# Optimization experiments

Hardware: AMD Instinct MI355X
Metric: run time of the kernel (lower is better)

The kernel has to match this reference:

```python
import jax, jax.numpy as jnp
import numpy as np

B, S, HID = 2, 2048, 4096
NUM_HEADS, NUM_KV_HEADS, HEAD_DIM = 32, 8, 128
KV_SIZE = HID * NUM_KV_HEADS // NUM_HEADS  # 1024


def setup_inputs() -> dict:
    key = jax.random.key(0)
    ks = jax.random.split(key, 5)
    x = jax.random.normal(ks[0], (B, S, HID), dtype=jnp.float32)
    wq = jax.random.normal(ks[1], (HID, HID), dtype=jnp.float32) * 0.02
    wk = jax.random.normal(ks[2], (HID, KV_SIZE), dtype=jnp.float32) * 0.02
    wv = jax.random.normal(ks[3], (HID, KV_SIZE), dtype=jnp.float32) * 0.02
    wo = jax.random.normal(ks[4], (KV_SIZE, HID), dtype=jnp.float32) * 0.02
    return {"x": x, "wq": wq, "wk": wk, "wv": wv, "wo": wo}


def reference(x, wq, wk, wv, wo):
    b, s, _ = x.shape
    g = NUM_HEADS // NUM_KV_HEADS  # num_head_groups
    q = x @ wq  # [b, s, hid]
    k = x @ wk  # [b, s, kv_size]
    v = x @ wv  # [b, s, kv_size]
    # 'b s (h d) -> b h s d' with h = num_heads
    q = q.reshape(b, s, NUM_HEADS, HEAD_DIM).transpose(0, 2, 1, 3)
    # 'b s (h d) -> b h d s' with h = num_kv_heads
    k = k.reshape(b, s, NUM_KV_HEADS, HEAD_DIM).transpose(0, 2, 3, 1)
    # 'b s (h d) -> b h s d'
    v = v.reshape(b, s, NUM_KV_HEADS, HEAD_DIM).transpose(0, 2, 1, 3)
    # 'b (h g) s d -> b g h s d' with g = num_head_groups, h = num_kv_heads
    q = q.reshape(b, NUM_KV_HEADS, g, s, HEAD_DIM).transpose(0, 2, 1, 3, 4)
    # NOTE: faithful to source - g is contracted (summed) here, it does not
    # appear in the output subscripts.
    scores = jnp.einsum('bghqd,bhdk->bhqk', q, k) / jnp.sqrt(
        jnp.asarray(HEAD_DIM, dtype=x.dtype))
    scores = jax.nn.softmax(scores, axis=-1)
    values = jnp.einsum('bhqk,bhkd->bhqd', scores, v)  # [b, h_kv, s, d]
    values = values.transpose(0, 2, 1, 3).reshape(b, s, KV_SIZE)
    return values @ wo  # [b, s, hid]
```

## Files before the change

kernel.cpp:

```cpp
#include <hip/hip_runtime.h>
#include <stdint.h>

#define S 2048
#define HID 4096
#define NKV 8
#define HD 128
#define KV 1024
#define BATCH 2
#define NQKV 3072
#define MROWS 4096

typedef __attribute__((ext_vector_type(4))) float f32x4;
typedef __attribute__((ext_vector_type(8))) __bf16 bf16x8;
typedef __attribute__((ext_vector_type(8))) unsigned short ushort8;
typedef __attribute__((ext_vector_type(4))) unsigned short ushort4_t;
typedef __attribute__((ext_vector_type(4))) float float4_t;

__device__ __forceinline__ unsigned short f2bf(float f) {
    unsigned int u = __builtin_bit_cast(unsigned int, f);
    u += 0x7fffu + ((u >> 16) & 1u);
    return (unsigned short)(u >> 16);
}
__device__ __forceinline__ float bf2f(unsigned short s) {
    unsigned int u = ((unsigned int)s) << 16;
    return __builtin_bit_cast(float, u);
}

__device__ __forceinline__ void gl2lds16(const void* g, void* l) {
    __builtin_amdgcn_global_load_lds(
        (const __attribute__((address_space(1))) void*)(uintptr_t)(g),
        (__attribute__((address_space(3))) void*)(uintptr_t)(l),
        16, 0, 0);
}

__global__ __launch_bounds__(256) void castx_kernel(const float* __restrict__ x,
                                                    unsigned short* __restrict__ xb) {
    int i = (blockIdx.x * 256 + threadIdx.x) * 4;
    float4_t v = *(const float4_t*)&x[i];
    ushort4_t o;
    o.x = f2bf(v.x); o.y = f2bf(v.y); o.z = f2bf(v.z); o.w = f2bf(v.w);
    *(ushort4_t*)&xb[i] = o;
}

__global__ __launch_bounds__(256) void wcat_kernel(const float* __restrict__ wq,
                                                   const float* __restrict__ wk,
                                                   const float* __restrict__ wv,
                                                   unsigned short* __restrict__ WcatT) {
    __shared__ float T[64 * 65];
    const int tid = threadIdx.x;
    const int k0 = blockIdx.x * 64;
    const int n0 = blockIdx.y * 64;
    const float scale = 0.088388347648318447f;
#pragma unroll
    for (int i = 0; i < 16; i++) {
        int kl = (tid >> 6) + i * 4;
        int nl = tid & 63;
        int k = k0 + kl, n = n0 + nl;
        float v;
        if (n < KV) {
            int kvh = n >> 7, d = n & 127;
            const float* p = wq + (size_t)k * HID + kvh * 512 + d;
            v = (p[0] + p[128] + p[256] + p[384]) * scale;
        } else if (n < 2048) {
            v = wk[(size_t)k * KV + (n - KV)];
        } else {
            v = wv[(size_t)k * KV + (n - 2048)];
        }
        T[kl * 65 + nl] = v;
    }
    __syncthreads();
#pragma unroll
    for (int i = 0; i < 16; i++) {
        int nl = (tid >> 6) + i * 4;
        int kl = tid & 63;
        WcatT[(size_t)(n0 + nl) * HID + k0 + kl] = f2bf(T[kl * 65 + nl]);
    }
}

__global__ __launch_bounds__(256) void wot_kernel(const float* __restrict__ wo,
                                                  unsigned short* __restrict__ woT) {
    __shared__ float T[64 * 65];
    const int tid = threadIdx.x;
    const int k0 = blockIdx.x * 64;
    const int n0 = blockIdx.y * 64;
#pragma unroll
    for (int i = 0; i < 16; i++) {
        int kl = (tid >> 6) + i * 4, nl = tid & 63;
        T[kl * 65 + nl] = wo[(size_t)(k0 + kl) * HID + n0 + nl];
    }
    __syncthreads();
#pragma unroll
    for (int i = 0; i < 16; i++) {
        int nl = (tid >> 6) + i * 4, kl = tid & 63;
        woT[(size_t)(n0 + nl) * KV + k0 + kl] = f2bf(T[kl * 65 + nl]);
    }
}

#define BAR() do { asm volatile("" ::: "memory"); __builtin_amdgcn_s_barrier(); asm volatile("" ::: "memory"); } while (0)
#define WAITV2() asm volatile("s_waitcnt vmcnt(2)" ::: "memory")

__device__ __forceinline__ void stage2(const unsigned short* __restrict__ g,
                                       size_t so0, size_t so1,
                                       unsigned short* lds, int tid) {
    gl2lds16(g + so0, lds + (size_t)tid * 8);
    gl2lds16(g + so1, lds + (size_t)(512 + tid) * 8);
}

template <int OUT_BF16>
__global__ __launch_bounds__(512, 2) void gemm_bt8(const unsigned short* __restrict__ A,
                                                   const unsigned short* __restrict__ Bt,
                                                   void* __restrict__ Cv,
                                                   int M, int N, int K) {
    __shared__ unsigned short As[2][2][8192];
    __shared__ unsigned short Bs[2][2][8192];
    const int tid = threadIdx.x;
    const int lane = tid & 63, wave = tid >> 6;
    const int lm = lane & 15, quad = lane >> 4;
    const int wm = wave >> 2;
    const int wn = wave & 3;
    const int wnh = wn >> 1;
    const int wnb = (wn & 1) * 4;

    const int nbx = gridDim.x;
    const int id = blockIdx.y * nbx + blockIdx.x;
    const int cpx = (nbx * gridDim.y) >> 3;
    const int sid = (id & 7) * cpx + (id >> 3);
    const int m0 = (sid / nbx) * 256;
    const int n0 = (sid % nbx) * 256;

    size_t so0, so1;
    {
#pragma unroll
        for (int i = 0; i < 2; i++) {
            int p = i * 512 + tid;
            int ps = p ^ (((p >> 5) & 1) << 1);
            int s = ps >> 6, w = ps & 63;
            int row = ((s >> 1) << 4) + (w >> 2);
            int kc = ((s & 1) << 5) + ((w & 3) << 3);
            size_t off = (size_t)row * K + kc;
            if (i == 0) so0 = off; else so1 = off;
        }
    }
    const unsigned short* Agb = A + (size_t)m0 * K;
    const unsigned short* Bgb = Bt + (size_t)n0 * K;
    const size_t hK = (size_t)128 * K;

    const int roff = lm * 32 + ((quad << 3) ^ (((lm >> 3) & 1) << 4));

#define LDA(mi, kk, BUF) a[(mi) & 3][kk] = *(const bf16x8*)&As[BUF][wm][(((mi) * 2 + (kk)) << 9) + roff]
#define LDB(ni, kk, BUF) b[ni][kk] = *(const bf16x8*)&Bs[BUF][wnh][(((wnb + (ni)) * 2 + (kk)) << 9) + roff]
#define RD_A_LO(BUF) { LDA(0,0,BUF); LDA(0,1,BUF); LDA(1,0,BUF); LDA(1,1,BUF); LDA(2,0,BUF); LDA(2,1,BUF); LDA(3,0,BUF); LDA(3,1,BUF); }
#define RD_A_HI(BUF) { LDA(4,0,BUF); LDA(4,1,BUF); LDA(5,0,BUF); LDA(5,1,BUF); LDA(6,0,BUF); LDA(6,1,BUF); LDA(7,0,BUF); LDA(7,1,BUF); }
#define RD_B_LO(BUF) { LDB(0,0,BUF); LDB(0,1,BUF); LDB(1,0,BUF); LDB(1,1,BUF); }
#define RD_B_HI(BUF) { LDB(2,0,BUF); LDB(2,1,BUF); LDB(3,0,BUF); LDB(3,1,BUF); }
#define MFMA_Q(MB, NB) do { \
    __builtin_amdgcn_s_setprio(1); \
    _Pragma("unroll") for (int i_ = 0; i_ < 4; i_++) \
    _Pragma("unroll") for (int j_ = 0; j_ < 2; j_++) \
    _Pragma("unroll") for (int k_ = 0; k_ < 2; k_++) \
        acc[(MB) + i_][(NB) + j_] = __builtin_amdgcn_mfma_f32_16x16x32_bf16( \
            a[i_][k_], b[(NB) + j_][k_], acc[(MB) + i_][(NB) + j_], 0, 0, 0); \
    __builtin_amdgcn_s_setprio(0); \
} while (0)

    f32x4 acc[8][4] = {};
    bf16x8 a[4][2], b[4][2];

    const int KT = K >> 6;
    const int NT = KT >> 1;

    stage2(Agb, so0, so1, &As[0][0][0], tid);
    stage2(Agb + hK, so0, so1, &As[0][1][0], tid);
    stage2(Bgb, so0, so1, &Bs[0][0][0], tid);
    stage2(Bgb + hK, so0, so1, &Bs[0][1][0], tid);
    stage2(Agb + 64, so0, so1, &As[1][0][0], tid);
    WAITV2();
    BAR();

    for (int t = 0; t < NT; ++t) {
        const int t1 = 2 * t + 1;
        int t2 = 2 * t + 2; if (t2 >= KT) t2 = KT - 1;
        int t3 = 2 * t + 3; if (t3 >= KT) t3 = KT - 1;
        const size_t k1 = (size_t)t1 * 64, k2 = (size_t)t2 * 64, k3 = (size_t)t3 * 64;

        RD_A_LO(0); RD_B_LO(0);
        stage2(Agb + hK + k1, so0, so1, &As[1][1][0], tid);
        BAR(); MFMA_Q(0, 0); BAR();

        RD_B_HI(0);
        stage2(Bgb + k1, so0, so1, &Bs[1][0][0], tid);
        BAR(); MFMA_Q(0, 2); BAR();

        RD_A_HI(0);
        stage2(Bgb + hK + k1, so0, so1, &Bs[1][1][0], tid);
        BAR(); MFMA_Q(4, 2); BAR();

        stage2(Agb + k2, so0, so1, &As[0][0][0], tid);
        BAR(); MFMA_Q(4, 0);
        WAITV2();
        BAR();

        RD_A_LO(1); RD_B_LO(1);
        stage2(Agb + hK + k2, so0, so1, &As[0][1][0], tid);
        BAR(); MFMA_Q(0, 0); BAR();

        RD_B_HI(1);
        stage2(Bgb + k2, so0, so1, &Bs[0][0][0], tid);
        BAR(); MFMA_Q(0, 2); BAR();

        RD_A_HI(1);
        stage2(Bgb + hK + k2, so0, so1, &Bs[0][1][0], tid);
        BAR(); MFMA_Q(4, 2); BAR();

        stage2(Agb + k3, so0, so1, &As[1][0][0], tid);
        BAR(); MFMA_Q(4, 0);
        WAITV2();
        BAR();
    }

    const int crow0 = m0 + wm * 128 + quad * 4;
    const int ccol0 = n0 + wn * 64 + lm;
#pragma unroll
    for (int mi = 0; mi < 8; mi++)
#pragma unroll
        for (int ni = 0; ni < 4; ni++)
#pragma unroll
            for (int r = 0; r < 4; r++) {
                const int row = crow0 + mi * 16 + r;
                const int col = ccol0 + ni * 16;
                if (OUT_BF16)
                    ((unsigned short*)Cv)[(size_t)row * N + col] = f2bf(acc[mi][ni][r]);
                else
                    ((float*)Cv)[(size_t)row * N + col] = acc[mi][ni][r];
            }
#undef LDA
#undef LDB
#undef RD_A_LO
#undef RD_A_HI
#undef RD_B_LO
#undef RD_B_HI
#undef MFMA_Q
}

__global__ __launch_bounds__(256) void vt_kernel(const unsigned short* __restrict__ QKV,
                                                 unsigned short* __restrict__ Vt) {
    __shared__ unsigned short T[128 * 136];
    const int tid = threadIdx.x;
    const int st = blockIdx.x;
    const int bh = blockIdx.y;
    const int b = bh >> 3, h = bh & 7;
#pragma unroll
    for (int it = 0; it < 8; it++) {
        int chunk = tid + it * 256;
        int s = chunk >> 4, cc = chunk & 15;
        ushort8 v = *(const ushort8*)&QKV[(size_t)(b * S + st * 128 + s) * NQKV + 2048 + h * HD + cc * 8];
        *(ushort8*)&T[s * 136 + cc * 8] = v;
    }
    __syncthreads();
#pragma unroll
    for (int it = 0; it < 8; it++) {
        int chunk = tid + it * 256;
        int d = chunk >> 4, scc = chunk & 15;
        ushort8 o;
#pragma unroll
        for (int j = 0; j < 8; j++) o[j] = T[(scc * 8 + j) * 136 + d];
        *(ushort8*)&Vt[(size_t)((b * NKV + h) * HD + d) * S + st * 128 + scc * 8] = o;
    }
}

__global__ __launch_bounds__(256, 1) void attn_kernel(const unsigned short* __restrict__ QKV,
                                                      const unsigned short* __restrict__ Vt,
                                                      unsigned short* __restrict__ Oout) {
    __shared__ unsigned short Ks[64 * 128];
    __shared__ unsigned short Vs[128 * 64];
    __shared__ unsigned short Ps[128 * 64];
    const int tid = threadIdx.x;
    const int lane = tid & 63, wave = tid >> 6;
    const int lm = lane & 15, quad = lane >> 4;
    const int sw = lm & 7;
    const int qt = blockIdx.x;
    const int h = blockIdx.y;
    const int b = blockIdx.z;
    const int qrow0 = qt * 128 + wave * 32;

    bf16x8 qf[2][4];
#pragma unroll
    for (int rt = 0; rt < 2; rt++)
#pragma unroll
        for (int ks = 0; ks < 4; ks++) {
            size_t off = (size_t)(b * S + qrow0 + rt * 16 + lm) * NQKV + h * HD + ks * 32 + quad * 8;
            qf[rt][ks] = *(const bf16x8*)&QKV[off];
        }

    float lsum[2][4] = {};
    f32x4 oacc[2][8] = {};

    const int krow = tid >> 2, kc4 = tid & 3;
    const int vrow = tid >> 1, vc2 = tid & 1;
    const unsigned short* Kg0 = QKV + (size_t)(b * S) * NQKV + KV + h * HD + kc4 * 32;
    const unsigned short* Vg0 = Vt + (size_t)((b * NKV + h) * HD + vrow) * S + vc2 * 32;

    ushort8 kreg[4], vreg[4];
    {
        const unsigned short* kg = Kg0 + (size_t)krow * NQKV;
        const unsigned short* vg = Vg0;
#pragma unroll
        for (int j = 0; j < 4; j++) kreg[j] = *(const ushort8*)(kg + j * 8);
#pragma unroll
        for (int j = 0; j < 4; j++) vreg[j] = *(const ushort8*)(vg + j * 8);
    }

    for (int kt = 0; kt < 32; kt++) {
        __syncthreads();
#pragma unroll
        for (int j = 0; j < 4; j++)
            *(ushort8*)&Ks[krow * 128 + ((kc4 * 4 + j) ^ (krow & 7)) * 8] = kreg[j];
#pragma unroll
        for (int j = 0; j < 4; j++)
            *(ushort8*)&Vs[vrow * 64 + ((vc2 * 4 + j) ^ (vrow & 7)) * 8] = vreg[j];
        __syncthreads();
        if (kt < 31) {
            const unsigned short* kg = Kg0 + (size_t)((kt + 1) * 64 + krow) * NQKV;
            const unsigned short* vg = Vg0 + (kt + 1) * 64;
#pragma unroll
            for (int j = 0; j < 4; j++) kreg[j] = *(const ushort8*)(kg + j * 8);
#pragma unroll
            for (int j = 0; j < 4; j++) vreg[j] = *(const ushort8*)(vg + j * 8);
        }

        f32x4 sc[2][4] = {};
#pragma unroll
        for (int ks = 0; ks < 4; ks++)
#pragma unroll
            for (int ct = 0; ct < 4; ct++) {
                bf16x8 kf = *(const bf16x8*)&Ks[(ct * 16 + lm) * 128 + ((ks * 4 + quad) ^ sw) * 8];
                sc[0][ct] = __builtin_amdgcn_mfma_f32_16x16x32_bf16(qf[0][ks], kf, sc[0][ct], 0, 0, 0);
                sc[1][ct] = __builtin_amdgcn_mfma_f32_16x16x32_bf16(qf[1][ks], kf, sc[1][ct], 0, 0, 0);
            }

#pragma unroll
        for (int rt = 0; rt < 2; rt++)
#pragma unroll
            for (int ct = 0; ct < 4; ct++)
#pragma unroll
                for (int r = 0; r < 4; r++) {
                    float p = __expf(fminf(sc[rt][ct][r], 60.f));
                    unsigned short pb = f2bf(p);
                    lsum[rt][r] += bf2f(pb);
                    int prow = wave * 32 + rt * 16 + quad * 4 + r;
                    int pcol = ct * 16 + lm;
                    Ps[prow * 64 + (((pcol >> 3) ^ (prow & 7)) * 8) + (pcol & 7)] = pb;
                }

#pragma unroll
        for (int ks = 0; ks < 2; ks++) {
            bf16x8 af0 = *(const bf16x8*)&Ps[(wave * 32 + lm) * 64 + ((ks * 4 + quad) ^ sw) * 8];
            bf16x8 af1 = *(const bf16x8*)&Ps[(wave * 32 + 16 + lm) * 64 + ((ks * 4 + quad) ^ sw) * 8];
#pragma unroll
            for (int dt = 0; dt < 8; dt++) {
                bf16x8 vf = *(const bf16x8*)&Vs[(dt * 16 + lm) * 64 + ((ks * 4 + quad) ^ sw) * 8];
                oacc[0][dt] = __builtin_amdgcn_mfma_f32_16x16x32_bf16(af0, vf, oacc[0][dt], 0, 0, 0);
                oacc[1][dt] = __builtin_amdgcn_mfma_f32_16x16x32_bf16(af1, vf, oacc[1][dt], 0, 0, 0);
            }
        }
    }

#pragma unroll
    for (int rt = 0; rt < 2; rt++)
#pragma unroll
        for (int r = 0; r < 4; r++) {
            float v = lsum[rt][r];
            v += __shfl_xor(v, 8);
            v += __shfl_xor(v, 4);
            v += __shfl_xor(v, 2);
            v += __shfl_xor(v, 1);
            lsum[rt][r] = v;
        }
#pragma unroll
    for (int rt = 0; rt < 2; rt++)
#pragma unroll
        for (int dt = 0; dt < 8; dt++)
#pragma unroll
            for (int r = 0; r < 4; r++) {
                int row = b * S + qt * 128 + wave * 32 + rt * 16 + quad * 4 + r;
                int col = h * HD + dt * 16 + lm;
                Oout[(size_t)row * KV + col] = f2bf(oacc[rt][dt][r] / lsum[rt][r]);
            }
}

extern "C" void kernel_launch(void* const* d_in, const int* in_sizes, int n_in,
                              void* d_out, int out_size, void* d_ws, size_t ws_size,
                              hipStream_t stream) {
    (void)in_sizes; (void)n_in; (void)out_size; (void)ws_size;
    const float* x  = (const float*)d_in[0];
    const float* wq = (const float*)d_in[1];
    const float* wk = (const float*)d_in[2];
    const float* wv = (const float*)d_in[3];
    const float* wo = (const float*)d_in[4];
    float* out = (float*)d_out;
    char* ws = (char*)d_ws;

    unsigned short* xb    = (unsigned short*)(ws);
    unsigned short* WcatT = (unsigned short*)(ws + 33554432);
    unsigned short* woT   = (unsigned short*)(ws + 33554432 + 25165824);
    unsigned short* QKV   = (unsigned short*)(ws + 67108864);
    unsigned short* Vt    = (unsigned short*)(ws);
    unsigned short* AttnO = (unsigned short*)(ws + 8388608);

    castx_kernel<<<16384, 256, 0, stream>>>(x, xb);
    wcat_kernel<<<dim3(64, 48), 256, 0, stream>>>(wq, wk, wv, WcatT);
    wot_kernel<<<dim3(16, 64), 256, 0, stream>>>(wo, woT);
    gemm_bt8<1><<<dim3(NQKV / 256, MROWS / 256), 512, 0, stream>>>(xb, WcatT, QKV, MROWS, NQKV, HID);
    vt_kernel<<<dim3(16, 16), 256, 0, stream>>>(QKV, Vt);
    attn_kernel<<<dim3(16, NKV, BATCH), 256, 0, stream>>>(QKV, Vt, AttnO);
    gemm_bt8<0><<<dim3(HID / 256, MROWS / 256), 512, 0, stream>>>(AttnO, woT, out, MROWS, HID, KV);
}
```

Baseline: 426.3 us.

## Reorder GEMM prefetch into half-tile stages and shrink attention query tile to 64 rows

The GEMM load schedule is reorganised so each stage issues the lo/hi halves of A and B across both 128-row halves, with a deeper prefetch (vmcnt(6)) so more global-to-LDS traffic is in flight while MFMAs run. Separately, the attention kernel now processes 64 query rows per block (16 per wave) instead of 128, which doubles the grid to 512 blocks and raises occupancy to 2 blocks per CU with a smaller P buffer. The cost is that each loaded K/V tile is reused by fewer query rows, so K/V traffic doubles, and the reordered wait counts must stay correct for the ring of LDS buffers.

```diff
diff --git a/kernel.cpp b/kernel.cpp
--- a/kernel.cpp
+++ b/kernel.cpp
@@ -97,14 +97,7 @@
 }
 
 #define BAR() do { asm volatile("" ::: "memory"); __builtin_amdgcn_s_barrier(); asm volatile("" ::: "memory"); } while (0)
-#define WAITV2() asm volatile("s_waitcnt vmcnt(2)" ::: "memory")
-
-__device__ __forceinline__ void stage2(const unsigned short* __restrict__ g,
-                                       size_t so0, size_t so1,
-                                       unsigned short* lds, int tid) {
-    gl2lds16(g + so0, lds + (size_t)tid * 8);
-    gl2lds16(g + so1, lds + (size_t)(512 + tid) * 8);
-}
+#define WAITV6() asm volatile("s_waitcnt vmcnt(6)" ::: "memory")
 
 template <int OUT_BF16>
 __global__ __launch_bounds__(512, 2) void gemm_bt8(const unsigned short* __restrict__ A,
@@ -144,6 +137,9 @@
     const unsigned short* Agb = A + (size_t)m0 * K;
     const unsigned short* Bgb = Bt + (size_t)n0 * K;
     const size_t hK = (size_t)128 * K;
+
+#define STLO(G, L) gl2lds16((G) + so0, (L) + (size_t)tid * 8)
+#define STHI(G, L) gl2lds16((G) + so1, (L) + (size_t)(512 + tid) * 8)
 
     const int roff = lm * 32 + ((quad << 3) ^ (((lm >> 3) & 1) << 4));
 
@@ -169,52 +165,54 @@
     const int KT = K >> 6;
     const int NT = KT >> 1;
 
-    stage2(Agb, so0, so1, &As[0][0][0], tid);
-    stage2(Agb + hK, so0, so1, &As[0][1][0], tid);
-    stage2(Bgb, so0, so1, &Bs[0][0][0], tid);
-    stage2(Bgb + hK, so0, so1, &Bs[0][1][0], tid);
-    stage2(Agb + 64, so0, so1, &As[1][0][0], tid);
-    WAITV2();
+    STLO(Agb, &As[0][0][0]); STLO(Agb + hK, &As[0][1][0]);
+    STHI(Agb, &As[0][0][0]); STHI(Agb + hK, &As[0][1][0]);
+    STLO(Bgb, &Bs[0][0][0]); STLO(Bgb + hK, &Bs[0][1][0]);
+    STHI(Bgb, &Bs[0][0][0]); STHI(Bgb + hK, &Bs[0][1][0]);
+    STLO(Agb + 64, &As[1][0][0]); STLO(Agb + hK + 64, &As[1][1][0]);
+    STLO(Bgb + 64, &Bs[1][0][0]); STLO(Bgb + hK + 64, &Bs[1][1][0]);
+    STHI(Bgb + 64, &Bs[1][0][0]); STHI(Bgb + hK + 64, &Bs[1][1][0]);
+    WAITV6();
     BAR();
 
     for (int t = 0; t < NT; ++t) {
-        const int t1 = 2 * t + 1;
-        int t2 = 2 * t + 2; if (t2 >= KT) t2 = KT - 1;
-        int t3 = 2 * t + 3; if (t3 >= KT) t3 = KT - 1;
-        const size_t k1 = (size_t)t1 * 64, k2 = (size_t)t2 * 64, k3 = (size_t)t3 * 64;
+        const size_t k1 = (size_t)(2 * t + 1) * 64;
+        int t2i = 2 * t + 2; if (t2i >= KT) t2i = KT - 1;
+        int t3i = 2 * t + 3; if (t3i >= KT) t3i = KT - 1;
+        const size_t k2 = (size_t)t2i * 64, k3 = (size_t)t3i * 64;
 
         RD_A_LO(0); RD_B_LO(0);
-        stage2(Agb + hK + k1, so0, so1, &As[1][1][0], tid);
+        STHI(Agb + k1, &As[1][0][0]); STHI(Agb + hK + k1, &As[1][1][0]);
         BAR(); MFMA_Q(0, 0); BAR();
 
         RD_B_HI(0);
-        stage2(Bgb + k1, so0, so1, &Bs[1][0][0], tid);
+        STLO(Agb + k2, &As[0][0][0]); STLO(Agb + hK + k2, &As[0][1][0]);
         BAR(); MFMA_Q(0, 2); BAR();
 
         RD_A_HI(0);
-        stage2(Bgb + hK + k1, so0, so1, &Bs[1][1][0], tid);
+        STLO(Bgb + k2, &Bs[0][0][0]); STLO(Bgb + hK + k2, &Bs[0][1][0]);
         BAR(); MFMA_Q(4, 2); BAR();
 
-        stage2(Agb + k2, so0, so1, &As[0][0][0], tid);
+        STHI(Bgb + k2, &Bs[0][0][0]); STHI(Bgb + hK + k2, &Bs[0][1][0]);
         BAR(); MFMA_Q(4, 0);
-        WAITV2();
+        WAITV6();
         BAR();
 
         RD_A_LO(1); RD_B_LO(1);
-        stage2(Agb + hK + k2, so0, so1, &As[0][1][0], tid);
+        STHI(Agb + k2, &As[0][0][0]); STHI(Agb + hK + k2, &As[0][1][0]);
         BAR(); MFMA_Q(0, 0); BAR();
 
         RD_B_HI(1);
-        stage2(Bgb + k2, so0, so1, &Bs[0][0][0], tid);
+        STLO(Agb + k3, &As[1][0][0]); STLO(Agb + hK + k3, &As[1][1][0]);
         BAR(); MFMA_Q(0, 2); BAR();
 
         RD_A_HI(1);
-        stage2(Bgb + hK + k2, so0, so1, &Bs[0][1][0], tid);
+        STLO(Bgb + k3, &Bs[1][0][0]); STLO(Bgb + hK + k3, &Bs[1][1][0]);
         BAR(); MFMA_Q(4, 2); BAR();
 
-        stage2(Agb + k3, so0, so1, &As[1][0][0], tid);
+        STHI(Bgb + k3, &Bs[1][0][0]); STHI(Bgb + hK + k3, &Bs[1][1][0]);
         BAR(); MFMA_Q(4, 0);
-        WAITV2();
+        WAITV6();
         BAR();
     }
 
@@ -240,6 +238,8 @@
 #undef RD_B_LO
 #undef RD_B_HI
 #undef MFMA_Q
+#undef STLO
+#undef STHI
 }
 
 __global__ __launch_bounds__(256) void vt_kernel(const unsigned short* __restrict__ QKV,
@@ -268,32 +268,30 @@
     }
 }
 
-__global__ __launch_bounds__(256, 1) void attn_kernel(const unsigned short* __restrict__ QKV,
+__global__ __launch_bounds__(256, 2) void attn_kernel(const unsigned short* __restrict__ QKV,
                                                       const unsigned short* __restrict__ Vt,
                                                       unsigned short* __restrict__ Oout) {
     __shared__ unsigned short Ks[64 * 128];
     __shared__ unsigned short Vs[128 * 64];
-    __shared__ unsigned short Ps[128 * 64];
+    __shared__ unsigned short Ps[64 * 64];
     const int tid = threadIdx.x;
     const int lane = tid & 63, wave = tid >> 6;
     const int lm = lane & 15, quad = lane >> 4;
     const int sw = lm & 7;
-    const int qt = blockIdx.x;
-    const int h = blockIdx.y;
+    const int h = blockIdx.x;
+    const int qt = blockIdx.y;
     const int b = blockIdx.z;
-    const int qrow0 = qt * 128 + wave * 32;
-
-    bf16x8 qf[2][4];
-#pragma unroll
-    for (int rt = 0; rt < 2; rt++)
-#pragma unroll
-        for (int ks = 0; ks < 4; ks++) {
-            size_t off = (size_t)(b * S + qrow0 + rt * 16 + lm) * NQKV + h * HD + ks * 32 + quad * 8;
-            qf[rt][ks] = *(const bf16x8*)&QKV[off];
-        }
-
-    float lsum[2][4] = {};
-    f32x4 oacc[2][8] = {};
+    const int qrow0 = qt * 64 + wave * 16;
+
+    bf16x8 qf[4];
+#pragma unroll
+    for (int ks = 0; ks < 4; ks++) {
+        size_t off = (size_t)(b * S + qrow0 + lm) * NQKV + h * HD + ks * 32 + quad * 8;
+        qf[ks] = *(const bf16x8*)&QKV[off];
+    }
+
+    float lsum[4] = {};
+    f32x4 oacc[8] = {};
 
     const int krow = tid >> 2, kc4 = tid & 3;
     const int vrow = tid >> 1, vc2 = tid & 1;
@@ -328,64 +326,55 @@
             for (int j = 0; j < 4; j++) vreg[j] = *(const ushort8*)(vg + j * 8);
         }
 
-        f32x4 sc[2][4] = {};
+        f32x4 sc[4] = {};
 #pragma unroll
         for (int ks = 0; ks < 4; ks++)
 #pragma unroll
             for (int ct = 0; ct < 4; ct++) {
                 bf16x8 kf = *(const bf16x8*)&Ks[(ct * 16 + lm) * 128 + ((ks * 4 + quad) ^ sw) * 8];
-                sc[0][ct] = __builtin_amdgcn_mfma_f32_16x16x32_bf16(qf[0][ks], kf, sc[0][ct], 0, 0, 0);
-                sc[1][ct] = __builtin_amdgcn_mfma_f32_16x16x32_bf16(qf[1][ks], kf, sc[1][ct], 0, 0, 0);
+                sc[ct] = __builtin_amdgcn_mfma_f32_16x16x32_bf16(qf[ks], kf, sc[ct], 0, 0, 0);
             }
 
 #pragma unroll
-        for (int rt = 0; rt < 2; rt++)
-#pragma unroll
-            for (int ct = 0; ct < 4; ct++)
-#pragma unroll
-                for (int r = 0; r < 4; r++) {
-                    float p = __expf(fminf(sc[rt][ct][r], 60.f));
-                    unsigned short pb = f2bf(p);
-                    lsum[rt][r] += bf2f(pb);
-                    int prow = wave * 32 + rt * 16 + quad * 4 + r;
-                    int pcol = ct * 16 + lm;
-                    Ps[prow * 64 + (((pcol >> 3) ^ (prow & 7)) * 8) + (pcol & 7)] = pb;
-                }
+        for (int ct = 0; ct < 4; ct++)
+#pragma unroll
+            for (int r = 0; r < 4; r++) {
+                float p = __expf(fminf(sc[ct][r], 60.f));
+                unsigned short pb = f2bf(p);
+                lsum[r] += bf2f(pb);
+                int prow = wave * 16 + quad * 4 + r;
+                int pcol = ct * 16 + lm;
+                Ps[prow * 64 + (((pcol >> 3) ^ (prow & 7)) * 8) + (pcol & 7)] = pb;
+            }
 
 #pragma unroll
         for (int ks = 0; ks < 2; ks++) {
-            bf16x8 af0 = *(const bf16x8*)&Ps[(wave * 32 + lm) * 64 + ((ks * 4 + quad) ^ sw) * 8];
-            bf16x8 af1 = *(const bf16x8*)&Ps[(wave * 32 + 16 + lm) * 64 + ((ks * 4 + quad) ^ sw) * 8];
+            bf16x8 af = *(const bf16x8*)&Ps[(wave * 16 + lm) * 64 + ((ks * 4 + quad) ^ sw) * 8];
 #pragma unroll
             for (int dt = 0; dt < 8; dt++) {
                 bf16x8 vf = *(const bf16x8*)&Vs[(dt * 16 + lm) * 64 + ((ks * 4 + quad) ^ sw) * 8];
-                oacc[0][dt] = __builtin_amdgcn_mfma_f32_16x16x32_bf16(af0, vf, oacc[0][dt], 0, 0, 0);
-                oacc[1][dt] = __builtin_amdgcn_mfma_f32_16x16x32_bf16(af1, vf, oacc[1][dt], 0, 0, 0);
+                oacc[dt] = __builtin_amdgcn_mfma_f32_16x16x32_bf16(af, vf, oacc[dt], 0, 0, 0);
             }
         }
     }
 
 #pragma unroll
-    for (int rt = 0; rt < 2; rt++)
+    for (int r = 0; r < 4; r++) {
+        float v = lsum[r];
+        v += __shfl_xor(v, 8);
+        v += __shfl_xor(v, 4);
+        v += __shfl_xor(v, 2);
+        v += __shfl_xor(v, 1);
+        lsum[r] = v;
+    }
+#pragma unroll
+    for (int dt = 0; dt < 8; dt++)
 #pragma unroll
         for (int r = 0; r < 4; r++) {
-            float v = lsum[rt][r];
-            v += __shfl_xor(v, 8);
-            v += __shfl_xor(v, 4);
-            v += __shfl_xor(v, 2);
-            v += __shfl_xor(v, 1);
-            lsum[rt][r] = v;
+            int row = b * S + qt * 64 + wave * 16 + quad * 4 + r;
+            int col = h * HD + dt * 16 + lm;
+            Oout[(size_t)row * KV + col] = f2bf(oacc[dt][r] / lsum[r]);
         }
-#pragma unroll
-    for (int rt = 0; rt < 2; rt++)
-#pragma unroll
-        for (int dt = 0; dt < 8; dt++)
-#pragma unroll
-            for (int r = 0; r < 4; r++) {
-                int row = b * S + qt * 128 + wave * 32 + rt * 16 + quad * 4 + r;
-                int col = h * HD + dt * 16 + lm;
-                Oout[(size_t)row * KV + col] = f2bf(oacc[rt][dt][r] / lsum[rt][r]);
-            }
 }
 
 extern "C" void kernel_launch(void* const* d_in, const int* in_sizes, int n_in,
@@ -412,6 +401,6 @@
     wot_kernel<<<dim3(16, 64), 256, 0, stream>>>(wo, woT);
     gemm_bt8<1><<<dim3(NQKV / 256, MROWS / 256), 512, 0, stream>>>(xb, WcatT, QKV, MROWS, NQKV, HID);
     vt_kernel<<<dim3(16, 16), 256, 0, stream>>>(QKV, Vt);
-    attn_kernel<<<dim3(16, NKV, BATCH), 256, 0, stream>>>(QKV, Vt, AttnO);
+    attn_kernel<<<dim3(NKV, 32, BATCH), 256, 0, stream>>>(QKV, Vt, AttnO);
     gemm_bt8<0><<<dim3(HID / 256, MROWS / 256), 512, 0, stream>>>(AttnO, woT, out, MROWS, HID, KV);
 }
```

New measurement: 423.3 us. Within noise of the previous version (-0.7%).
